# Kernel tuning notes

Measured on AMD Instinct MI355X. Metric: run time of the kernel, lower is better.

## Reference

```python
import jax, jax.numpy as jnp
import numpy as np

B, T, N_EMBD, HEAD = 4, 4096, 1024, 64


def setup_inputs() -> dict:
    key = jax.random.key(0)
    kx, kk, kq, kv = jax.random.split(key, 4)
    x = jax.random.normal(kx, (B, T, N_EMBD), dtype=jnp.float32)
    s = 1.0 / np.sqrt(N_EMBD)  # init scale so activations stay O(1)
    Wk = jax.random.normal(kk, (N_EMBD, HEAD), dtype=jnp.float32) * s
    Wq = jax.random.normal(kq, (N_EMBD, HEAD), dtype=jnp.float32) * s
    Wv = jax.random.normal(kv, (N_EMBD, HEAD), dtype=jnp.float32) * s
    return {"x": x, "Wk": Wk, "Wq": Wq, "Wv": Wv}


def reference(x, Wk, Wq, Wv):
    Bd, Td, C = x.shape
    k = jnp.einsum('btc,ch->bth', x, Wk)
    q = jnp.einsum('btc,ch->bth', x, Wq)
    v = jnp.einsum('btc,ch->bth', x, Wv)
    # scores scaled by C**-0.5 where C = n_embd (as in the source, not head_size)
    w = jnp.einsum('bth,bsh->bts', q, k) * (C ** -0.5)
    causal = jnp.tril(jnp.ones((Td, Td), dtype=bool))  # [T, T]
    w = jnp.where(causal, w, -jnp.inf)
    w = jax.nn.softmax(w, axis=-1)
    out = jnp.einsum('bts,bsh->bth', w, v)  # [B, T, head_size]
    return out
```

## Files before the change

kernel.cpp:

```cpp
#include <hip/hip_runtime.h>
#include <cmath>

#define NB 4
#define NT 4096
#define NC 1024
#define NH 64
#define SCALE 0.03125f
#define MFIX 3.0f
#define LOG2E 1.4426950408889634f
#define QE 1048576

typedef __attribute__((ext_vector_type(8))) short v8s;
typedef __attribute__((ext_vector_type(4))) float f32x4;

static __device__ __forceinline__ ushort f2bf(float x) {
    union { float f; uint u; } c; c.f = x;
    return (ushort)((c.u + 0x7FFF + ((c.u >> 16) & 1)) >> 16);
}
static __device__ __forceinline__ uint pk2bf(float hi_f, float lo_f) {
    uint uh = __float_as_uint(hi_f) + 0x8000u;
    uint ul = __float_as_uint(lo_f) + 0x8000u;
    return __builtin_amdgcn_perm(uh, ul, 0x07060302u);
}

__global__ __launch_bounds__(256) void prep_kernel(
    const float* __restrict__ Wk, const float* __restrict__ Wq,
    const float* __restrict__ Wv, ushort* __restrict__ Wb)
{
    const int g    = blockIdx.x * 256 + threadIdx.x;
    const int lane = g & 63;
    const int kc   = (g >> 6) & 31;
    const int nt   = g >> 11;
    const int n    = nt * 16 + (lane & 15);
    const float* W = (n < 64) ? Wq : (n < 128) ? Wk : Wv;
    const int col  = n & 63;
    const int k0   = kc * 32 + ((lane >> 4) << 3);
    ushort t8[8];
    #pragma unroll
    for (int j = 0; j < 8; ++j)
        t8[j] = f2bf(W[(k0 + j) * 64 + col]);
    *(uint4*)(Wb + (size_t)g * 8) = *(const uint4*)t8;
}

#define PPAD 72

__global__ __launch_bounds__(256) void proj_kernel(
    const float* __restrict__ x, const ushort* __restrict__ Wb,
    ushort* __restrict__ qpack, ushort* __restrict__ kpack,
    ushort* __restrict__ vpack)
{
    __shared__ __align__(16) ushort As[2][32 * PPAD];
    __shared__ __align__(16) ushort Cs[32][200];

    const int tid  = threadIdx.x;
    const int w    = tid >> 6;
    const int lane = tid & 63;
    const int ln   = lane & 15;
    const int quad = lane >> 4;
    const long r0  = (long)blockIdx.x * 32;

    const int arow = tid >> 3, acol = (tid & 7) * 8;
    const float* xs = x + (r0 + arow) * NC + acol;

    const ushort* wb0 = Wb + (size_t)(w * 3 + 0) * 16384 + lane * 8;
    const ushort* wb1 = Wb + (size_t)(w * 3 + 1) * 16384 + lane * 8;
    const ushort* wb2 = Wb + (size_t)(w * 3 + 2) * 16384 + lane * 8;

    f32x4 acc[2][3];
    #pragma unroll
    for (int s = 0; s < 2; ++s)
        #pragma unroll
        for (int nt = 0; nt < 3; ++nt) acc[s][nt] = (f32x4){0.f,0.f,0.f,0.f};

    float4 f0 = *(const float4*)(xs);
    float4 f1 = *(const float4*)(xs + 4);
    float4 g0 = *(const float4*)(xs + 64);
    float4 g1 = *(const float4*)(xs + 68);
    v8s b[3][2];
    b[0][0] = *(const v8s*)(wb0);       b[0][1] = *(const v8s*)(wb0 + 512);
    b[1][0] = *(const v8s*)(wb1);       b[1][1] = *(const v8s*)(wb1 + 512);
    b[2][0] = *(const v8s*)(wb2);       b[2][1] = *(const v8s*)(wb2 + 512);
    {
        uint4 p = { pk2bf(f0.y, f0.x), pk2bf(f0.w, f0.z),
                    pk2bf(f1.y, f1.x), pk2bf(f1.w, f1.z) };
        *(uint4*)(&As[0][arow * PPAD + acol]) = p;
    }
    __syncthreads();

    int buf = 0;
    #pragma unroll
    for (int it = 0; it < 16; ++it) {
        float4 h0, h1;
        v8s nb[3][2];
        if (it < 14) {
            const int k2 = (it + 2) * 64;
            h0 = *(const float4*)(xs + k2);
            h1 = *(const float4*)(xs + k2 + 4);
        }
        if (it < 15) {
            const int off = (it + 1) * 1024;
            nb[0][0] = *(const v8s*)(wb0 + off); nb[0][1] = *(const v8s*)(wb0 + off + 512);
            nb[1][0] = *(const v8s*)(wb1 + off); nb[1][1] = *(const v8s*)(wb1 + off + 512);
            nb[2][0] = *(const v8s*)(wb2 + off); nb[2][1] = *(const v8s*)(wb2 + off + 512);
        }

        #pragma unroll
        for (int s = 0; s < 2; ++s) {
            const ushort* ap = &As[buf][(s * 16 + ln) * PPAD + quad * 8];
            v8s a0 = *(const v8s*)(ap);
            v8s a1 = *(const v8s*)(ap + 32);
            #pragma unroll
            for (int nt = 0; nt < 3; ++nt) {
                acc[s][nt] = __builtin_amdgcn_mfma_f32_16x16x32_bf16(a0, b[nt][0], acc[s][nt], 0, 0, 0);
                acc[s][nt] = __builtin_amdgcn_mfma_f32_16x16x32_bf16(a1, b[nt][1], acc[s][nt], 0, 0, 0);
            }
        }

        if (it < 15) {
            uint4 p = { pk2bf(g0.y, g0.x), pk2bf(g0.w, g0.z),
                        pk2bf(g1.y, g1.x), pk2bf(g1.w, g1.z) };
            *(uint4*)(&As[buf ^ 1][arow * PPAD + acol]) = p;
            #pragma unroll
            for (int nt = 0; nt < 3; ++nt) {
                b[nt][0] = nb[nt][0];
                b[nt][1] = nb[nt][1];
            }
        }
        if (it < 14) { g0 = h0; g1 = h1; }
        __syncthreads();
        buf ^= 1;
    }

    #pragma unroll
    for (int s = 0; s < 2; ++s)
        #pragma unroll
        for (int nt = 0; nt < 3; ++nt)
            #pragma unroll
            for (int r = 0; r < 4; ++r)
                Cs[s * 16 + quad * 4 + r][(w * 3 + nt) * 16 + ln] = f2bf(acc[s][nt][r]);
    __syncthreads();

    const int b_blk = (int)(r0 >> 12);
    const int t_loc = (int)(r0 & 4095);
    const int kt    = t_loc >> 6;
    const int kcb   = (t_loc >> 5) & 1;
    const int qt16a = t_loc >> 4;

    {
        const int f = tid >> 6, sx = f >> 1, kc = f & 1, lp = tid & 63;
        const int lnp = lp & 15, qdp = lp >> 4;
        const size_t fid = ((size_t)(b_blk * 256 + qt16a + sx) * 2 + kc);
        uint4 uq = *(const uint4*)(&Cs[sx * 16 + lnp][kc * 32 + qdp * 8]);
        *(uint4*)(qpack + fid * 512 + lp * 8) = uq;
        uint4 uk = *(const uint4*)(&Cs[sx * 16 + lnp][64 + kc * 32 + qdp * 8]);
        *(uint4*)(kpack + fid * 512 + lp * 8) = uk;
    }
    {
        const int td = tid >> 6, lp = tid & 63;
        const int lnv = lp & 15, qg = lp >> 4;
        ushort t8[8];
        #pragma unroll
        for (int j = 0; j < 8; ++j)
            t8[j] = Cs[qg * 8 + j][128 + td * 16 + lnv];
        const size_t fv = ((size_t)(b_blk * 64 + kt) * 2 + kcb) * 4 + td;
        *(uint4*)(vpack + fv * 512 + lp * 8) = *(const uint4*)t8;
    }
}

#define LPAD 40

__global__ __launch_bounds__(256) void attn_kernel(
    const ushort* __restrict__ qpack, const ushort* __restrict__ kpack,
    const ushort* __restrict__ vpack, float* __restrict__ out)
{
    __shared__ __align__(16) ushort Ps[4][32 * LPAD];
    __shared__ __align__(16) float Obuf[4][32][68];
    __shared__ float Lbuf[4][32];

    const int id = blockIdx.x;
    const int j  = id >> 2;
    const int b  = id & 3;

    const int tid  = threadIdx.x;
    const int w    = tid >> 6;
    const int lane = tid & 63;
    const int ln   = lane & 15;
    const int quad = lane >> 4;

    const ushort* qpb = qpack + (size_t)b * 256 * 2 * 512 + lane * 8;
    const ushort* kpb = kpack + (size_t)b * 256 * 2 * 512 + lane * 8;
    const ushort* vpb = vpack + (size_t)b * 128 * 4 * 512 + lane * 8;

    ushort* Pw = &Ps[w][0];

    #pragma unroll
    for (int ph = 0; ph < 2; ++ph) {
        const int jp = ph ? (127 - j) : j;
        const int q0 = jp * 32;

        v8s qf[2][2];
        #pragma unroll
        for (int s = 0; s < 2; ++s) {
            qf[s][0] = *(const v8s*)(qpb + ((size_t)((jp * 2 + s) * 2 + 0)) * 512);
            qf[s][1] = *(const v8s*)(qpb + ((size_t)((jp * 2 + s) * 2 + 1)) * 512);
        }

        f32x4 o[2][4];
        #pragma unroll
        for (int s = 0; s < 2; ++s)
            #pragma unroll
            for (int td = 0; td < 4; ++td) o[s][td] = (f32x4){0.f,0.f,0.f,0.f};
        float l[2] = {0.f, 0.f};

        for (int kk = w; kk <= jp; kk += 4) {
            const ushort* kfb = kpb + (size_t)kk * 4 * 512;
            const ushort* vfb = vpb + (size_t)kk * 4 * 512;
            const bool diag = (kk == jp);

            #pragma unroll
            for (int tk = 0; tk < 2; ++tk) {
                v8s kf0 = *(const v8s*)(kfb + (tk * 2 + 0) * 512);
                v8s kf1 = *(const v8s*)(kfb + (tk * 2 + 1) * 512);
                const int keybase = kk * 32 + tk * 16 + quad * 4;
                #pragma unroll
                for (int s = 0; s < 2; ++s) {
                    f32x4 acc = (f32x4){0.f,0.f,0.f,0.f};
                    acc = __builtin_amdgcn_mfma_f32_16x16x32_bf16(kf0, qf[s][0], acc, 0, 0, 0);
                    acc = __builtin_amdgcn_mfma_f32_16x16x32_bf16(kf1, qf[s][1], acc, 0, 0, 0);
                    const int qg = q0 + s * 16 + ln;
                    float p[4];
                    #pragma unroll
                    for (int r = 0; r < 4; ++r) {
                        float e = fmaf(acc[r], SCALE * LOG2E, -MFIX * LOG2E);
                        if (diag && (keybase + r > qg)) e = -1e30f;
                        p[r] = __builtin_amdgcn_exp2f(e);
                        l[s] += p[r];
                    }
                    uint2 pw = { pk2bf(p[1], p[0]), pk2bf(p[3], p[2]) };
                    *(uint2*)(&Pw[(s * 16 + ln) * LPAD + tk * 16 + quad * 4]) = pw;
                }
            }

            v8s vf[4];
            #pragma unroll
            for (int td = 0; td < 4; ++td)
                vf[td] = *(const v8s*)(vfb + td * 512);
            #pragma unroll
            for (int s = 0; s < 2; ++s) {
                v8s pf = *(const v8s*)(&Pw[(s * 16 + ln) * LPAD + quad * 8]);
                #pragma unroll
                for (int td = 0; td < 4; ++td)
                    o[s][td] = __builtin_amdgcn_mfma_f32_16x16x32_bf16(pf, vf[td], o[s][td], 0, 0, 0);
            }
        }

        #pragma unroll
        for (int s = 0; s < 2; ++s) {
            l[s] += __shfl_xor(l[s], 16);
            l[s] += __shfl_xor(l[s], 32);
        }

        #pragma unroll
        for (int s = 0; s < 2; ++s) {
            #pragma unroll
            for (int td = 0; td < 4; ++td)
                #pragma unroll
                for (int r = 0; r < 4; ++r)
                    Obuf[w][s * 16 + quad * 4 + r][td * 16 + ln] = o[s][td][r];
            if (quad == 0) Lbuf[w][s * 16 + ln] = l[s];
        }
        __syncthreads();

        {
            const int qr = tid >> 3;
            const int h0 = (tid & 7) * 8;
            float s0=0.f,s1=0.f,s2=0.f,s3=0.f,s4=0.f,s5=0.f,s6=0.f,s7=0.f,Ls=0.f;
            #pragma unroll
            for (int ww = 0; ww < 4; ++ww) {
                const float* Or = &Obuf[ww][qr][h0];
                float4 u = *(const float4*)(Or);
                float4 v2 = *(const float4*)(Or + 4);
                s0 += u.x;  s1 += u.y;  s2 += u.z;  s3 += u.w;
                s4 += v2.x; s5 += v2.y; s6 += v2.z; s7 += v2.w;
                Ls += Lbuf[ww][qr];
            }
            const float inv = 1.0f / Ls;
            float4 r0 = { s0 * inv, s1 * inv, s2 * inv, s3 * inv };
            float4 r1 = { s4 * inv, s5 * inv, s6 * inv, s7 * inv };
            float* ob = out + ((size_t)b * NT + q0 + qr) * NH + h0;
            *(float4*)(ob)     = r0;
            *(float4*)(ob + 4) = r1;
        }
        __syncthreads();
    }
}

extern "C" void kernel_launch(void* const* d_in, const int* in_sizes, int n_in,
                              void* d_out, int out_size, void* d_ws, size_t ws_size,
                              hipStream_t stream)
{
    const float* x  = (const float*)d_in[0];
    const float* Wk = (const float*)d_in[1];
    const float* Wq = (const float*)d_in[2];
    const float* Wv = (const float*)d_in[3];
    float* out = (float*)d_out;

    char* wsb = (char*)d_ws;
    ushort* qpack = (ushort*)wsb;
    ushort* kpack = qpack + QE;
    ushort* vpack = kpack + QE;
    ushort* Wb    = vpack + QE;

    prep_kernel<<<96, 256, 0, stream>>>(Wk, Wq, Wv, Wb);
    proj_kernel<<<NB * NT / 32, 256, 0, stream>>>(x, Wb, qpack, kpack, vpack);
    attn_kernel<<<64 * NB, 256, 0, stream>>>(qpack, kpack, vpack, out);
}
```

Baseline: 137.5 us.

## Grow attention blocks to 16 waves and reduce partial outputs in two stages

Each attention block now runs 1024 threads (16 waves) instead of 256, so key tiles are split across 16 waves per query tile rather than 4. The cross-wave reduction becomes two-stage: waves 8-15 write partials to shared memory, waves 0-7 add them in, then all threads do a final 8-way sum and store. The aim is more parallelism across the 256 blocks, which on their own underfill the GPU. In exchange there is an extra barrier, narrower stores, and possible register pressure under the 1024 launch bound.

Measured after the change: 129.9 us. 5.5% less time.

```diff
diff --git a/kernel.cpp b/kernel.cpp
--- a/kernel.cpp
+++ b/kernel.cpp
@@ -169,13 +169,13 @@
 
 #define LPAD 40
 
-__global__ __launch_bounds__(256) void attn_kernel(
+__global__ __launch_bounds__(1024) void attn_kernel(
     const ushort* __restrict__ qpack, const ushort* __restrict__ kpack,
     const ushort* __restrict__ vpack, float* __restrict__ out)
 {
-    __shared__ __align__(16) ushort Ps[4][32 * LPAD];
-    __shared__ __align__(16) float Obuf[4][32][68];
-    __shared__ float Lbuf[4][32];
+    __shared__ __align__(16) ushort Ps[16][32 * LPAD];
+    __shared__ __align__(16) float Obuf[8][32][68];
+    __shared__ float Lbuf[8][32];
 
     const int id = blockIdx.x;
     const int j  = id >> 2;
@@ -212,7 +212,7 @@
             for (int td = 0; td < 4; ++td) o[s][td] = (f32x4){0.f,0.f,0.f,0.f};
         float l[2] = {0.f, 0.f};
 
-        for (int kk = w; kk <= jp; kk += 4) {
+        for (int kk = w; kk <= jp; kk += 16) {
             const ushort* kfb = kpb + (size_t)kk * 4 * 512;
             const ushort* vfb = vpb + (size_t)kk * 4 * 512;
             const bool diag = (kk == jp);
@@ -260,36 +260,48 @@
             l[s] += __shfl_xor(l[s], 32);
         }
 
-        #pragma unroll
-        for (int s = 0; s < 2; ++s) {
-            #pragma unroll
-            for (int td = 0; td < 4; ++td)
+        if (w >= 8) {
+            #pragma unroll
+            for (int s = 0; s < 2; ++s) {
                 #pragma unroll
-                for (int r = 0; r < 4; ++r)
-                    Obuf[w][s * 16 + quad * 4 + r][td * 16 + ln] = o[s][td][r];
-            if (quad == 0) Lbuf[w][s * 16 + ln] = l[s];
+                for (int td = 0; td < 4; ++td)
+                    #pragma unroll
+                    for (int r = 0; r < 4; ++r)
+                        Obuf[w - 8][s * 16 + quad * 4 + r][td * 16 + ln] = o[s][td][r];
+                if (quad == 0) Lbuf[w - 8][s * 16 + ln] = l[s];
+            }
         }
         __syncthreads();
 
+        if (w < 8) {
+            #pragma unroll
+            for (int s = 0; s < 2; ++s) {
+                l[s] += Lbuf[w][s * 16 + ln];
+                #pragma unroll
+                for (int td = 0; td < 4; ++td)
+                    #pragma unroll
+                    for (int r = 0; r < 4; ++r) {
+                        float m = o[s][td][r] + Obuf[w][s * 16 + quad * 4 + r][td * 16 + ln];
+                        Obuf[w][s * 16 + quad * 4 + r][td * 16 + ln] = m;
+                    }
+                if (quad == 0) Lbuf[w][s * 16 + ln] = l[s];
+            }
+        }
+        __syncthreads();
+
         {
-            const int qr = tid >> 3;
-            const int h0 = (tid & 7) * 8;
-            float s0=0.f,s1=0.f,s2=0.f,s3=0.f,s4=0.f,s5=0.f,s6=0.f,s7=0.f,Ls=0.f;
-            #pragma unroll
-            for (int ww = 0; ww < 4; ++ww) {
+            const int qr = tid >> 5;
+            const int h0 = (tid & 31) * 2;
+            float s0 = 0.f, s1 = 0.f, Ls = 0.f;
+            #pragma unroll
+            for (int ww = 0; ww < 8; ++ww) {
                 const float* Or = &Obuf[ww][qr][h0];
-                float4 u = *(const float4*)(Or);
-                float4 v2 = *(const float4*)(Or + 4);
-                s0 += u.x;  s1 += u.y;  s2 += u.z;  s3 += u.w;
-                s4 += v2.x; s5 += v2.y; s6 += v2.z; s7 += v2.w;
+                s0 += Or[0]; s1 += Or[1];
                 Ls += Lbuf[ww][qr];
             }
             const float inv = 1.0f / Ls;
-            float4 r0 = { s0 * inv, s1 * inv, s2 * inv, s3 * inv };
-            float4 r1 = { s4 * inv, s5 * inv, s6 * inv, s7 * inv };
-            float* ob = out + ((size_t)b * NT + q0 + qr) * NH + h0;
-            *(float4*)(ob)     = r0;
-            *(float4*)(ob + 4) = r1;
+            float2 r = { s0 * inv, s1 * inv };
+            *(float2*)(out + ((size_t)b * NT + q0 + qr) * NH + h0) = r;
         }
         __syncthreads();
     }
@@ -313,5 +325,5 @@
 
     prep_kernel<<<96, 256, 0, stream>>>(Wk, Wq, Wv, Wb);
     proj_kernel<<<NB * NT / 32, 256, 0, stream>>>(x, Wb, qpack, kpack, vpack);
-    attn_kernel<<<64 * NB, 256, 0, stream>>>(qpack, kpack, vpack, out);
-}
+    attn_kernel<<<64 * NB, 1024, 0, stream>>>(qpack, kpack, vpack, out);
+}
```
